# Kernel tuning notes

Measured on AMD Instinct MI355X. Metric: run time of the kernel, lower is better.

## Reference

```python
import jax, jax.numpy as jnp
import numpy as np

T, D, H, E, K = 8192, 1024, 4096, 8, 2


def setup_inputs() -> dict:
    key = jax.random.key(0)
    ks = jax.random.split(key, 6)
    s_in = 1.0 / np.sqrt(D)
    s_hid = 1.0 / np.sqrt(H)
    return {
        "hidden_states": jax.random.normal(ks[0], (T, D), dtype=jnp.float32),
        "router_w": jax.random.normal(ks[1], (D, E), dtype=jnp.float32) * s_in,
        "expert_w1": jax.random.normal(ks[2], (E, D, H), dtype=jnp.float32) * s_in,
        "expert_w2": jax.random.normal(ks[3], (E, H, D), dtype=jnp.float32) * s_hid,
        "shared_w1": jax.random.normal(ks[4], (D, H), dtype=jnp.float32) * s_in,
        "shared_w2": jax.random.normal(ks[5], (H, D), dtype=jnp.float32) * s_hid,
    }


def reference(hidden_states, router_w, expert_w1, expert_w2, shared_w1, shared_w2):
    x = hidden_states  # [T, D]
    # --- router: softmax over experts, keep top-k, renormalize ---
    probs = jax.nn.softmax(x @ router_w, axis=-1)            # [T, E]
    top_v, top_i = jax.lax.top_k(probs, K)                   # [T, K]
    top_v = top_v / jnp.sum(top_v, axis=-1, keepdims=True)
    # dense combine weights [T, E]; zero for non-selected experts
    comb = jnp.zeros((x.shape[0], E), x.dtype).at[
        jnp.arange(x.shape[0])[:, None], top_i].set(top_v)
    # --- routed experts (dense reference for grouped GEMM) ---
    h = jax.nn.silu(jnp.einsum('td,edh->eth', x, expert_w1))  # [E, T, H]
    eo = jnp.einsum('eth,ehd->etd', h, expert_w2)             # [E, T, D]
    routed = jnp.einsum('te,etd->td', comb, eo)               # [T, D]
    # --- shared expert, always active ---
    shared = jax.nn.silu(x @ shared_w1) @ shared_w2           # [T, D]
    return routed + shared
```

## Files before the change

kernel.cpp:

```cpp
#include <hip/hip_runtime.h>
#include <hip/hip_bf16.h>
#include <stdint.h>

typedef unsigned short u16;
typedef __attribute__((ext_vector_type(8))) short bf16x8;
typedef __attribute__((ext_vector_type(4))) float f32x4;

constexpr int T_ = 8192;
constexpr int D_ = 1024;
constexpr int H_ = 4096;
constexpr int E_ = 8;
constexpr int MAXROWS = 25600;
constexpr int NTILES  = 200;

__device__ __forceinline__ unsigned int f2bf_bits(float f) {
  unsigned int u = __float_as_uint(f);
  return (u + 0x7fffu + ((u >> 16) & 1u)) >> 16;
}

__device__ __forceinline__ void load_lds16(const void* g, void* s) {
  __builtin_amdgcn_global_load_lds(
      (const __attribute__((address_space(1))) unsigned int*)g,
      (__attribute__((address_space(3))) unsigned int*)s, 16, 0, 0);
}

__global__ __launch_bounds__(256) void router_kernel(
    const float* __restrict__ x, const float* __restrict__ rw,
    int* __restrict__ counts, int* __restrict__ tok2, float* __restrict__ wgt2) {
  __shared__ float rw_s[E_ * D_];
  __shared__ int c_s[E_];
  const int tid = threadIdx.x;
  if (tid < E_) c_s[tid] = 0;
  for (int f = tid; f < 2048; f += 256) {
    int d = f >> 1, p = f & 1;
    float4 v = *(const float4*)(rw + d * 8 + p * 4);
    rw_s[(p * 4 + 0) * D_ + d] = v.x;
    rw_s[(p * 4 + 1) * D_ + d] = v.y;
    rw_s[(p * 4 + 2) * D_ + d] = v.z;
    rw_s[(p * 4 + 3) * D_ + d] = v.w;
  }
  __syncthreads();
  const int wid = tid >> 6, lane = tid & 63;
  for (int ti = 0; ti < 16; ++ti) {
    const int t = blockIdx.x * 64 + wid * 16 + ti;
    const float* xr = x + (long)t * D_;
    float acc[E_] = {0.f, 0.f, 0.f, 0.f, 0.f, 0.f, 0.f, 0.f};
    for (int j = 0; j < 16; ++j) {
      const int d = lane + 64 * j;
      const float xv = xr[d];
#pragma unroll
      for (int e = 0; e < E_; ++e) acc[e] += xv * rw_s[e * D_ + d];
    }
#pragma unroll
    for (int off = 32; off >= 1; off >>= 1) {
#pragma unroll
      for (int e = 0; e < E_; ++e) acc[e] += __shfl_xor(acc[e], off, 64);
    }
    if (lane == 0) {
      int i0 = 0; float l0 = acc[0];
#pragma unroll
      for (int e = 1; e < E_; ++e) if (acc[e] > l0) { l0 = acc[e]; i0 = e; }
      int i1 = -1; float l1 = -3.4e38f;
#pragma unroll
      for (int e = 0; e < E_; ++e) if (e != i0 && acc[e] > l1) { l1 = acc[e]; i1 = e; }
      const float r = __expf(l1 - l0);
      const float inv = 1.f / (1.f + r);
      tok2[2 * t] = i0; tok2[2 * t + 1] = i1;
      wgt2[2 * t] = inv; wgt2[2 * t + 1] = r * inv;
      atomicAdd(&c_s[i0], 1); atomicAdd(&c_s[i1], 1);
    }
  }
  __syncthreads();
  if (tid < E_) atomicAdd(&counts[tid], c_s[tid]);
}

__global__ void scan_kernel(const int* __restrict__ counts, int* __restrict__ offs,
                            int* __restrict__ tile_expert, int* __restrict__ rowtok) {
  __shared__ int so[10];
  const int tid = threadIdx.x;
  if (tid == 0) {
    int o = 0;
    for (int e = 0; e < E_; ++e) { so[e] = o; o += ((counts[e] + 127) >> 7) << 7; }
    so[8] = o;
    o += T_;
    so[9] = o;
    for (int i = 0; i < 10; ++i) offs[i] = so[i];
  }
  __syncthreads();
  for (int i = tid; i < NTILES; i += 256) {
    const int row = i << 7;
    int e = 8;
    if (row < so[8]) {
      e = 7;
      for (int k = 0; k < 7; ++k) if (row < so[k + 1]) { e = k; break; }
    }
    tile_expert[i] = e;
  }
  for (int r = tid; r < MAXROWS; r += 256) rowtok[r] = 0;
}

__global__ __launch_bounds__(256) void assign_kernel(
    const int* __restrict__ tok2, const int* __restrict__ offs,
    int* __restrict__ cursors, int* __restrict__ rowtok, int* __restrict__ pos2) {
  __shared__ int lcnt[E_], lbase[E_];
  const int tid = threadIdx.x;
  if (tid < E_) lcnt[tid] = 0;
  __syncthreads();
  const int t = blockIdx.x * 256 + tid;
  const int e0 = tok2[2 * t], e1 = tok2[2 * t + 1];
  const int s0 = atomicAdd(&lcnt[e0], 1);
  const int s1 = atomicAdd(&lcnt[e1], 1);
  __syncthreads();
  if (tid < E_) lbase[tid] = offs[tid] + atomicAdd(&cursors[tid], lcnt[tid]);
  __syncthreads();
  const int p0 = lbase[e0] + s0, p1 = lbase[e1] + s1;
  rowtok[p0] = t; rowtok[p1] = t;
  pos2[2 * t] = p0; pos2[2 * t + 1] = p1;
  rowtok[offs[8] + t] = t;
}

__global__ __launch_bounds__(256) void cvt_x_kernel(const float* __restrict__ x,
                                                    u16* __restrict__ xb) {
  const long i = ((long)blockIdx.x * 256 + threadIdx.x) * 4;
  const float4 v = *(const float4*)(x + i);
  ushort4 o;
  o.x = (u16)f2bf_bits(v.x); o.y = (u16)f2bf_bits(v.y);
  o.z = (u16)f2bf_bits(v.z); o.w = (u16)f2bf_bits(v.w);
  *(ushort4*)(xb + i) = o;
}

__global__ __launch_bounds__(256) void transpose_cvt_kernel(
    const float* __restrict__ src8, const float* __restrict__ srcShared,
    u16* __restrict__ dst, int R, int C) {
  __shared__ float tile[64][65];
  const long stride = (long)R * C;
  const float* src = (blockIdx.z < 8) ? src8 + (long)blockIdx.z * stride : srcShared;
  u16* d = dst + (long)blockIdx.z * stride;
  const int tid = threadIdx.x;
  const int r0 = blockIdx.y * 64, c0 = blockIdx.x * 64;
  const int lr = tid >> 4, lc4 = tid & 15;
#pragma unroll
  for (int p = 0; p < 4; ++p) {
    const float4 v = *(const float4*)(src + (long)(r0 + lr + 16 * p) * C + c0 + lc4 * 4);
    tile[lr + 16 * p][lc4 * 4 + 0] = v.x;
    tile[lr + 16 * p][lc4 * 4 + 1] = v.y;
    tile[lr + 16 * p][lc4 * 4 + 2] = v.z;
    tile[lr + 16 * p][lc4 * 4 + 3] = v.w;
  }
  __syncthreads();
#pragma unroll
  for (int p = 0; p < 4; ++p) {
    const int rr = lr + 16 * p;
    ushort4 o;
    o.x = (u16)f2bf_bits(tile[lc4 * 4 + 0][rr]);
    o.y = (u16)f2bf_bits(tile[lc4 * 4 + 1][rr]);
    o.z = (u16)f2bf_bits(tile[lc4 * 4 + 2][rr]);
    o.w = (u16)f2bf_bits(tile[lc4 * 4 + 3][rr]);
    *(ushort4*)(d + (long)(c0 + rr) * R + r0 + lc4 * 4) = o;
  }
}

template <bool G1, int CHM>
__global__ __launch_bounds__(256) void moe_gemm(
    const u16* __restrict__ A, const u16* __restrict__ Bt, void* __restrict__ C,
    const int* __restrict__ rowtok, const int* __restrict__ tile_expert) {
  constexpr int K = G1 ? 1024 : 4096;
  constexpr int N = G1 ? 4096 : 1024;
  constexpr int NT = N / 128;
  __shared__ u16 As[2 * 4096];
  __shared__ u16 Bs[2 * 4096];

  const int tid = threadIdx.x;
  int mt, nt;
  {
    const int bid = blockIdx.x;
    const int cb = CHM * NT;
    const int chunk = bid / cb;
    const int mt0 = chunk * CHM;
    const int m = min(CHM, NTILES - mt0);
    const int rem = bid - chunk * cb;
    mt = mt0 + rem % m;
    nt = rem / m;
  }
  const int e = tile_expert[mt];

  const int sr = tid >> 2;
  const int sc = (tid & 3) << 3;

  long aoff0, aoff1;
  if constexpr (G1) {
    aoff0 = (long)rowtok[mt * 128 + sr] * K;
    aoff1 = (long)rowtok[mt * 128 + 64 + sr] * K;
  } else {
    aoff0 = (long)(mt * 128 + sr) * K;
    aoff1 = (long)(mt * 128 + 64 + sr) * K;
  }
  const u16* pa0 = A + aoff0 + sc;
  const u16* pa1 = A + aoff1 + sc;
  const u16* pb0 = Bt + (long)e * N * K + (long)(nt * 128 + sr) * K + sc;
  const u16* pb1 = pb0 + (long)64 * K;

  u16* sA0[2] = {As + tid * 8, As + 4096 + tid * 8};
  u16* sA1[2] = {As + 2048 + tid * 8, As + 4096 + 2048 + tid * 8};
  u16* sB0[2] = {Bs + tid * 8, Bs + 4096 + tid * 8};
  u16* sB1[2] = {Bs + 2048 + tid * 8, Bs + 4096 + 2048 + tid * 8};

  const int lane = tid & 63;
  const int wid = tid >> 6;
  const int wm = (wid >> 1) * 64;
  const int wn = (wid & 1) * 64;
  const int lr = lane & 15;
  const int quad = lane >> 4;

  f32x4 acc[4][4] = {};

  load_lds16(pa0, sA0[0]);
  load_lds16(pa1, sA1[0]);
  load_lds16(pb0, sB0[0]);
  load_lds16(pb1, sB1[0]);

#pragma unroll 1
  for (int k0 = 0; k0 < K; k0 += 64) {
    __syncthreads();
    if (k0 + 32 < K) {
      load_lds16(pa0 + k0 + 32, sA0[1]);
      load_lds16(pa1 + k0 + 32, sA1[1]);
      load_lds16(pb0 + k0 + 32, sB0[1]);
      load_lds16(pb1 + k0 + 32, sB1[1]);
    }
    {
      bf16x8 af[4], bfv[4];
#pragma unroll
      for (int i = 0; i < 4; ++i)
        af[i] = *(const bf16x8*)(As + (wm + i * 16 + lr) * 32 + quad * 8);
#pragma unroll
      for (int j = 0; j < 4; ++j)
        bfv[j] = *(const bf16x8*)(Bs + (wn + j * 16 + lr) * 32 + quad * 8);
#pragma unroll
      for (int i = 0; i < 4; ++i)
#pragma unroll
        for (int j = 0; j < 4; ++j)
          acc[i][j] = __builtin_amdgcn_mfma_f32_16x16x32_bf16(af[i], bfv[j], acc[i][j], 0, 0, 0);
    }
    __syncthreads();
    if (k0 + 64 < K) {
      load_lds16(pa0 + k0 + 64, sA0[0]);
      load_lds16(pa1 + k0 + 64, sA1[0]);
      load_lds16(pb0 + k0 + 64, sB0[0]);
      load_lds16(pb1 + k0 + 64, sB1[0]);
    }
    {
      bf16x8 af[4], bfv[4];
#pragma unroll
      for (int i = 0; i < 4; ++i)
        af[i] = *(const bf16x8*)(As + 4096 + (wm + i * 16 + lr) * 32 + quad * 8);
#pragma unroll
      for (int j = 0; j < 4; ++j)
        bfv[j] = *(const bf16x8*)(Bs + 4096 + (wn + j * 16 + lr) * 32 + quad * 8);
#pragma unroll
      for (int i = 0; i < 4; ++i)
#pragma unroll
        for (int j = 0; j < 4; ++j)
          acc[i][j] = __builtin_amdgcn_mfma_f32_16x16x32_bf16(af[i], bfv[j], acc[i][j], 0, 0, 0);
    }
  }

  const int rbase = mt * 128 + wm + quad * 4;
  if constexpr (G1) {
    u16* Hout = (u16*)C;
#pragma unroll
    for (int i = 0; i < 4; ++i) {
#pragma unroll
      for (int j = 0; j < 4; ++j) {
#pragma unroll
        for (int r = 0; r < 4; ++r) {
          float v = acc[i][j][r];
          v = v / (1.f + __expf(-v));
          unsigned int u = f2bf_bits(v);
          unsigned int other = (unsigned int)__shfl_xor((int)u, 1, 64);
          if (!(lane & 1)) {
            const unsigned int w = (u & 0xffffu) | (other << 16);
            const long row = rbase + i * 16 + r;
            const int col = nt * 128 + wn + j * 16 + lr;
            *(unsigned int*)(Hout + row * N + col) = w;
          }
        }
      }
    }
  } else {
    float* O = (float*)C;
#pragma unroll
    for (int i = 0; i < 4; ++i)
#pragma unroll
      for (int j = 0; j < 4; ++j)
#pragma unroll
        for (int r = 0; r < 4; ++r) {
          const long row = rbase + i * 16 + r;
          const int col = nt * 128 + wn + j * 16 + lr;
          O[row * N + col] = acc[i][j][r];
        }
  }
}

__global__ __launch_bounds__(256) void combine_kernel(
    const float* __restrict__ eo, const int* __restrict__ pos2,
    const float* __restrict__ wgt2, const int* __restrict__ offs,
    float* __restrict__ out) {
  const int t = blockIdx.x, tid = threadIdx.x;
  const int p0 = pos2[2 * t], p1 = pos2[2 * t + 1];
  const float w0 = wgt2[2 * t], w1 = wgt2[2 * t + 1];
  const int ps = offs[8] + t;
  const long c = (long)tid * 4;
  const float4 a = *(const float4*)(eo + (long)p0 * D_ + c);
  const float4 b = *(const float4*)(eo + (long)p1 * D_ + c);
  const float4 s = *(const float4*)(eo + (long)ps * D_ + c);
  float4 o;
  o.x = w0 * a.x + w1 * b.x + s.x;
  o.y = w0 * a.y + w1 * b.y + s.y;
  o.z = w0 * a.z + w1 * b.z + s.z;
  o.w = w0 * a.w + w1 * b.w + s.w;
  *(float4*)(out + (long)t * D_ + c) = o;
}

extern "C" void kernel_launch(void* const* d_in, const int* in_sizes, int n_in,
                              void* d_out, int out_size, void* d_ws, size_t ws_size,
                              hipStream_t stream) {
  const float* x   = (const float*)d_in[0];
  const float* rw  = (const float*)d_in[1];
  const float* w1  = (const float*)d_in[2];
  const float* w2  = (const float*)d_in[3];
  const float* sw1 = (const float*)d_in[4];
  const float* sw2 = (const float*)d_in[5];
  float* out = (float*)d_out;

  char* ws = (char*)d_ws;
  int*   counts      = (int*)(ws + 0);
  int*   cursors     = (int*)(ws + 64);
  int*   offs        = (int*)(ws + 128);
  int*   tile_expert = (int*)(ws + 192);
  int*   tok2        = (int*)(ws + 4096);
  float* wgt2        = (float*)(ws + 4096 + 65536);
  int*   pos2        = (int*)(ws + 4096 + 131072);
  int*   rowtok      = (int*)(ws + 4096 + 196608);

  size_t off = 1u << 20;
  u16* xb  = (u16*)(ws + off); off += (size_t)T_ * D_ * 2;
  u16* w1t = (u16*)(ws + off); off += (size_t)9 * H_ * D_ * 2;
  u16* w2t = (u16*)(ws + off); off += (size_t)9 * D_ * H_ * 2;
  u16* h   = (u16*)(ws + off); off += (size_t)MAXROWS * H_ * 2;
  float* eo = (float*)(ws + off); off += (size_t)MAXROWS * D_ * 4;

  hipMemsetAsync(ws, 0, 256, stream);
  router_kernel<<<128, 256, 0, stream>>>(x, rw, counts, tok2, wgt2);
  scan_kernel<<<1, 256, 0, stream>>>(counts, offs, tile_expert, rowtok);
  assign_kernel<<<32, 256, 0, stream>>>(tok2, offs, cursors, rowtok, pos2);
  cvt_x_kernel<<<T_ * D_ / 1024, 256, 0, stream>>>(x, xb);
  transpose_cvt_kernel<<<dim3(H_ / 64, D_ / 64, 9), 256, 0, stream>>>(w1, sw1, w1t, D_, H_);
  transpose_cvt_kernel<<<dim3(D_ / 64, H_ / 64, 9), 256, 0, stream>>>(w2, sw2, w2t, H_, D_);
  moe_gemm<true, 24><<<NTILES * (H_ / 128), 256, 0, stream>>>(xb, w1t, h, rowtok, tile_expert);
  moe_gemm<false, 64><<<NTILES * (D_ / 128), 256, 0, stream>>>(h, w2t, eo, rowtok, tile_expert);
  combine_kernel<<<T_, 256, 0, stream>>>(eo, pos2, wgt2, offs, out);
}
```

Before: 1.092 ms.

## Enlarge MoE GEMM M-tile to 256 rows and store expert outputs as bf16

The grouped GEMM now computes 256x128 tiles, with each wave holding 8x4 MFMA accumulators, and experts are padded to 256-row multiples. Unused trailing tiles are marked -1 and exit early. The LDS staging layout is reorganised so fragment reads are contiguous per lane, and launch bounds request two blocks per CU. The second GEMM writes bf16 instead of fp32 and the combine kernel converts back, which halves output traffic at the cost of precision. The larger tiles also add register pressure and padding waste.

```diff
diff --git a/kernel.cpp b/kernel.cpp
--- a/kernel.cpp
+++ b/kernel.cpp
@@ -10,12 +10,15 @@
 constexpr int D_ = 1024;
 constexpr int H_ = 4096;
 constexpr int E_ = 8;
-constexpr int MAXROWS = 25600;
-constexpr int NTILES  = 200;
+constexpr int NT_M  = 104;
+constexpr int MAXR  = NT_M * 256;
 
 __device__ __forceinline__ unsigned int f2bf_bits(float f) {
   unsigned int u = __float_as_uint(f);
   return (u + 0x7fffu + ((u >> 16) & 1u)) >> 16;
+}
+__device__ __forceinline__ float bf2f(u16 b) {
+  return __uint_as_float(((unsigned int)b) << 16);
 }
 
 __device__ __forceinline__ void load_lds16(const void* g, void* s) {
@@ -80,23 +83,27 @@
   const int tid = threadIdx.x;
   if (tid == 0) {
     int o = 0;
-    for (int e = 0; e < E_; ++e) { so[e] = o; o += ((counts[e] + 127) >> 7) << 7; }
+    for (int e = 0; e < E_; ++e) { so[e] = o; o += ((counts[e] + 255) >> 8) << 8; }
     so[8] = o;
     o += T_;
     so[9] = o;
     for (int i = 0; i < 10; ++i) offs[i] = so[i];
   }
   __syncthreads();
-  for (int i = tid; i < NTILES; i += 256) {
-    const int row = i << 7;
-    int e = 8;
+  for (int i = tid; i < NT_M; i += 256) {
+    const int row = i << 8;
+    int e;
     if (row < so[8]) {
       e = 7;
       for (int k = 0; k < 7; ++k) if (row < so[k + 1]) { e = k; break; }
+    } else if (row < so[9]) {
+      e = 8;
+    } else {
+      e = -1;
     }
     tile_expert[i] = e;
   }
-  for (int r = tid; r < MAXROWS; r += 256) rowtok[r] = 0;
+  for (int r = tid; r < MAXR; r += 256) rowtok[r] = 0;
 }
 
 __global__ __launch_bounds__(256) void assign_kernel(
@@ -161,149 +168,135 @@
 }
 
 template <bool G1, int CHM>
-__global__ __launch_bounds__(256) void moe_gemm(
-    const u16* __restrict__ A, const u16* __restrict__ Bt, void* __restrict__ C,
+__global__ __launch_bounds__(256, 2) void moe_gemm(
+    const u16* __restrict__ A, const u16* __restrict__ Bt, u16* __restrict__ C,
     const int* __restrict__ rowtok, const int* __restrict__ tile_expert) {
   constexpr int K = G1 ? 1024 : 4096;
   constexpr int N = G1 ? 4096 : 1024;
-  constexpr int NT = N / 128;
-  __shared__ u16 As[2 * 4096];
+  constexpr int NTn = N / 128;
+  __shared__ u16 As[2 * 8192];
   __shared__ u16 Bs[2 * 4096];
 
   const int tid = threadIdx.x;
   int mt, nt;
   {
     const int bid = blockIdx.x;
-    const int cb = CHM * NT;
+    const int cb = CHM * NTn;
     const int chunk = bid / cb;
     const int mt0 = chunk * CHM;
-    const int m = min(CHM, NTILES - mt0);
+    const int m = min(CHM, NT_M - mt0);
     const int rem = bid - chunk * cb;
     mt = mt0 + rem % m;
     nt = rem / m;
   }
   const int e = tile_expert[mt];
-
-  const int sr = tid >> 2;
-  const int sc = (tid & 3) << 3;
-
-  long aoff0, aoff1;
-  if constexpr (G1) {
-    aoff0 = (long)rowtok[mt * 128 + sr] * K;
-    aoff1 = (long)rowtok[mt * 128 + 64 + sr] * K;
-  } else {
-    aoff0 = (long)(mt * 128 + sr) * K;
-    aoff1 = (long)(mt * 128 + 64 + sr) * K;
-  }
-  const u16* pa0 = A + aoff0 + sc;
-  const u16* pa1 = A + aoff1 + sc;
-  const u16* pb0 = Bt + (long)e * N * K + (long)(nt * 128 + sr) * K + sc;
-  const u16* pb1 = pb0 + (long)64 * K;
-
-  u16* sA0[2] = {As + tid * 8, As + 4096 + tid * 8};
-  u16* sA1[2] = {As + 2048 + tid * 8, As + 4096 + 2048 + tid * 8};
-  u16* sB0[2] = {Bs + tid * 8, Bs + 4096 + tid * 8};
-  u16* sB1[2] = {Bs + 2048 + tid * 8, Bs + 4096 + 2048 + tid * 8};
+  if (e < 0) return;
+
+  const int ric   = ((tid >> 6) << 4) | (tid & 15);
+  const int sc    = ((tid >> 4) & 3) << 3;
+
+  const u16* pa[4];
+#pragma unroll
+  for (int c = 0; c < 4; ++c) {
+    const int grow = mt * 256 + c * 64 + ric;
+    const long arow = G1 ? (long)rowtok[grow] : (long)grow;
+    pa[c] = A + arow * K + sc;
+  }
+  const u16* pb[2];
+#pragma unroll
+  for (int c = 0; c < 2; ++c)
+    pb[c] = Bt + (long)e * N * K + (long)(nt * 128 + c * 64 + ric) * K + sc;
 
   const int lane = tid & 63;
   const int wid = tid >> 6;
-  const int wm = (wid >> 1) * 64;
-  const int wn = (wid & 1) * 64;
+  const int wmh = wid >> 1;
+  const int wnh = wid & 1;
+  const int wm = wmh * 128, wn = wnh * 64;
   const int lr = lane & 15;
   const int quad = lane >> 4;
-
-  f32x4 acc[4][4] = {};
-
-  load_lds16(pa0, sA0[0]);
-  load_lds16(pa1, sA1[0]);
-  load_lds16(pb0, sB0[0]);
-  load_lds16(pb1, sB1[0]);
+  const int lane8 = lane * 8;
+
+  f32x4 acc[8][4] = {};
+
+#pragma unroll
+  for (int c = 0; c < 4; ++c) load_lds16(pa[c], As + c * 2048 + tid * 8);
+#pragma unroll
+  for (int c = 0; c < 2; ++c) load_lds16(pb[c], Bs + c * 2048 + tid * 8);
 
 #pragma unroll 1
   for (int k0 = 0; k0 < K; k0 += 64) {
     __syncthreads();
     if (k0 + 32 < K) {
-      load_lds16(pa0 + k0 + 32, sA0[1]);
-      load_lds16(pa1 + k0 + 32, sA1[1]);
-      load_lds16(pb0 + k0 + 32, sB0[1]);
-      load_lds16(pb1 + k0 + 32, sB1[1]);
+#pragma unroll
+      for (int c = 0; c < 4; ++c)
+        load_lds16(pa[c] + k0 + 32, As + 8192 + c * 2048 + tid * 8);
+#pragma unroll
+      for (int c = 0; c < 2; ++c)
+        load_lds16(pb[c] + k0 + 32, Bs + 4096 + c * 2048 + tid * 8);
     }
     {
-      bf16x8 af[4], bfv[4];
-#pragma unroll
-      for (int i = 0; i < 4; ++i)
-        af[i] = *(const bf16x8*)(As + (wm + i * 16 + lr) * 32 + quad * 8);
+      bf16x8 af[8], bfv[4];
 #pragma unroll
       for (int j = 0; j < 4; ++j)
-        bfv[j] = *(const bf16x8*)(Bs + (wn + j * 16 + lr) * 32 + quad * 8);
-#pragma unroll
-      for (int i = 0; i < 4; ++i)
+        bfv[j] = *(const bf16x8*)(Bs + wnh * 2048 + j * 512 + lane8);
+#pragma unroll
+      for (int i = 0; i < 8; ++i)
+        af[i] = *(const bf16x8*)(As + wmh * 4096 + i * 512 + lane8);
+#pragma unroll
+      for (int i = 0; i < 8; ++i)
 #pragma unroll
         for (int j = 0; j < 4; ++j)
           acc[i][j] = __builtin_amdgcn_mfma_f32_16x16x32_bf16(af[i], bfv[j], acc[i][j], 0, 0, 0);
     }
     __syncthreads();
     if (k0 + 64 < K) {
-      load_lds16(pa0 + k0 + 64, sA0[0]);
-      load_lds16(pa1 + k0 + 64, sA1[0]);
-      load_lds16(pb0 + k0 + 64, sB0[0]);
-      load_lds16(pb1 + k0 + 64, sB1[0]);
+#pragma unroll
+      for (int c = 0; c < 4; ++c)
+        load_lds16(pa[c] + k0 + 64, As + c * 2048 + tid * 8);
+#pragma unroll
+      for (int c = 0; c < 2; ++c)
+        load_lds16(pb[c] + k0 + 64, Bs + c * 2048 + tid * 8);
     }
     {
-      bf16x8 af[4], bfv[4];
-#pragma unroll
-      for (int i = 0; i < 4; ++i)
-        af[i] = *(const bf16x8*)(As + 4096 + (wm + i * 16 + lr) * 32 + quad * 8);
+      bf16x8 af[8], bfv[4];
 #pragma unroll
       for (int j = 0; j < 4; ++j)
-        bfv[j] = *(const bf16x8*)(Bs + 4096 + (wn + j * 16 + lr) * 32 + quad * 8);
-#pragma unroll
-      for (int i = 0; i < 4; ++i)
+        bfv[j] = *(const bf16x8*)(Bs + 4096 + wnh * 2048 + j * 512 + lane8);
+#pragma unroll
+      for (int i = 0; i < 8; ++i)
+        af[i] = *(const bf16x8*)(As + 8192 + wmh * 4096 + i * 512 + lane8);
+#pragma unroll
+      for (int i = 0; i < 8; ++i)
 #pragma unroll
         for (int j = 0; j < 4; ++j)
           acc[i][j] = __builtin_amdgcn_mfma_f32_16x16x32_bf16(af[i], bfv[j], acc[i][j], 0, 0, 0);
     }
   }
 
-  const int rbase = mt * 128 + wm + quad * 4;
-  if constexpr (G1) {
-    u16* Hout = (u16*)C;
-#pragma unroll
-    for (int i = 0; i < 4; ++i) {
-#pragma unroll
-      for (int j = 0; j < 4; ++j) {
-#pragma unroll
-        for (int r = 0; r < 4; ++r) {
-          float v = acc[i][j][r];
-          v = v / (1.f + __expf(-v));
-          unsigned int u = f2bf_bits(v);
-          unsigned int other = (unsigned int)__shfl_xor((int)u, 1, 64);
-          if (!(lane & 1)) {
-            const unsigned int w = (u & 0xffffu) | (other << 16);
-            const long row = rbase + i * 16 + r;
-            const int col = nt * 128 + wn + j * 16 + lr;
-            *(unsigned int*)(Hout + row * N + col) = w;
-          }
+  const int rbase = mt * 256 + wm + quad * 4;
+#pragma unroll
+  for (int i = 0; i < 8; ++i) {
+#pragma unroll
+    for (int j = 0; j < 4; ++j) {
+#pragma unroll
+      for (int r = 0; r < 4; ++r) {
+        float v = acc[i][j][r];
+        if constexpr (G1) v = v / (1.f + __expf(-v));
+        unsigned int u = f2bf_bits(v);
+        unsigned int other = (unsigned int)__shfl_xor((int)u, 1, 64);
+        if (!(lane & 1)) {
+          const unsigned int w = (u & 0xffffu) | (other << 16);
+          const long row = rbase + i * 16 + r;
+          const int col = nt * 128 + wn + j * 16 + lr;
+          *(unsigned int*)(C + row * N + col) = w;
         }
       }
     }
-  } else {
-    float* O = (float*)C;
-#pragma unroll
-    for (int i = 0; i < 4; ++i)
-#pragma unroll
-      for (int j = 0; j < 4; ++j)
-#pragma unroll
-        for (int r = 0; r < 4; ++r) {
-          const long row = rbase + i * 16 + r;
-          const int col = nt * 128 + wn + j * 16 + lr;
-          O[row * N + col] = acc[i][j][r];
-        }
   }
 }
 
 __global__ __launch_bounds__(256) void combine_kernel(
-    const float* __restrict__ eo, const int* __restrict__ pos2,
+    const u16* __restrict__ eo, const int* __restrict__ pos2,
     const float* __restrict__ wgt2, const int* __restrict__ offs,
     float* __restrict__ out) {
   const int t = blockIdx.x, tid = threadIdx.x;
@@ -311,14 +304,14 @@
   const float w0 = wgt2[2 * t], w1 = wgt2[2 * t + 1];
   const int ps = offs[8] + t;
   const long c = (long)tid * 4;
-  const float4 a = *(const float4*)(eo + (long)p0 * D_ + c);
-  const float4 b = *(const float4*)(eo + (long)p1 * D_ + c);
-  const float4 s = *(const float4*)(eo + (long)ps * D_ + c);
+  const ushort4 a = *(const ushort4*)(eo + (long)p0 * D_ + c);
+  const ushort4 b = *(const ushort4*)(eo + (long)p1 * D_ + c);
+  const ushort4 s = *(const ushort4*)(eo + (long)ps * D_ + c);
   float4 o;
-  o.x = w0 * a.x + w1 * b.x + s.x;
-  o.y = w0 * a.y + w1 * b.y + s.y;
-  o.z = w0 * a.z + w1 * b.z + s.z;
-  o.w = w0 * a.w + w1 * b.w + s.w;
+  o.x = w0 * bf2f(a.x) + w1 * bf2f(b.x) + bf2f(s.x);
+  o.y = w0 * bf2f(a.y) + w1 * bf2f(b.y) + bf2f(s.y);
+  o.z = w0 * bf2f(a.z) + w1 * bf2f(b.z) + bf2f(s.z);
+  o.w = w0 * bf2f(a.w) + w1 * bf2f(b.w) + bf2f(s.w);
   *(float4*)(out + (long)t * D_ + c) = o;
 }
 
@@ -337,7 +330,7 @@
   int*   counts      = (int*)(ws + 0);
   int*   cursors     = (int*)(ws + 64);
   int*   offs        = (int*)(ws + 128);
-  int*   tile_expert = (int*)(ws + 192);
+  int*   tile_expert = (int*)(ws + 512);
   int*   tok2        = (int*)(ws + 4096);
   float* wgt2        = (float*)(ws + 4096 + 65536);
   int*   pos2        = (int*)(ws + 4096 + 131072);
@@ -347,8 +340,8 @@
   u16* xb  = (u16*)(ws + off); off += (size_t)T_ * D_ * 2;
   u16* w1t = (u16*)(ws + off); off += (size_t)9 * H_ * D_ * 2;
   u16* w2t = (u16*)(ws + off); off += (size_t)9 * D_ * H_ * 2;
-  u16* h   = (u16*)(ws + off); off += (size_t)MAXROWS * H_ * 2;
-  float* eo = (float*)(ws + off); off += (size_t)MAXROWS * D_ * 4;
+  u16* h   = (u16*)(ws + off); off += (size_t)MAXR * H_ * 2;
+  u16* eo  = (u16*)(ws + off); off += (size_t)MAXR * D_ * 2;
 
   hipMemsetAsync(ws, 0, 256, stream);
   router_kernel<<<128, 256, 0, stream>>>(x, rw, counts, tok2, wgt2);
@@ -357,7 +350,7 @@
   cvt_x_kernel<<<T_ * D_ / 1024, 256, 0, stream>>>(x, xb);
   transpose_cvt_kernel<<<dim3(H_ / 64, D_ / 64, 9), 256, 0, stream>>>(w1, sw1, w1t, D_, H_);
   transpose_cvt_kernel<<<dim3(D_ / 64, H_ / 64, 9), 256, 0, stream>>>(w2, sw2, w2t, H_, D_);
-  moe_gemm<true, 24><<<NTILES * (H_ / 128), 256, 0, stream>>>(xb, w1t, h, rowtok, tile_expert);
-  moe_gemm<false, 64><<<NTILES * (D_ / 128), 256, 0, stream>>>(h, w2t, eo, rowtok, tile_expert);
+  moe_gemm<true, 16><<<NT_M * (H_ / 128), 256, 0, stream>>>(xb, w1t, h, rowtok, tile_expert);
+  moe_gemm<false, 16><<<NT_M * (D_ / 128), 256, 0, stream>>>(h, w2t, eo, rowtok, tile_expert);
   combine_kernel<<<T_, 256, 0, stream>>>(eo, pos2, wgt2, offs, out);
 }
```

After: 1.239 ms. 1.14x slower.
